# Optimization experiments

Measured on AMD Instinct MI355X. Metric: run time of the kernel, lower is better.

Reference implementation:

```python
import jax, jax.numpy as jnp
import numpy as np

NUM_EXPERTS = 8
GROUP_SIZE = 2
NUM_GROUPS = NUM_EXPERTS // GROUP_SIZE
NUM_SLOTS = 128
HIDDEN = 2048
D_FF = int(HIDDEN * 4 * (2.0 / 3.0))  # 5461
BATCH = 4
SEQ = 2048
BS = BATCH * SEQ


def setup_inputs() -> dict:
    key = jax.random.key(0)
    k0, k1, k2, k3 = jax.random.split(key, 4)
    x = jax.random.normal(k0, (BS, HIDDEN), dtype=jnp.float32)
    router_weights = jax.random.normal(k1, (BS, NUM_EXPERTS), dtype=jnp.float32)
    up_w = jax.random.normal(k2, (NUM_GROUPS, HIDDEN, D_FF), dtype=jnp.float32) * np.float32(1.0 / np.sqrt(HIDDEN))
    up_b = jnp.zeros((NUM_GROUPS, D_FF), dtype=jnp.float32)
    down_w = jax.random.normal(k3, (NUM_EXPERTS, D_FF, HIDDEN), dtype=jnp.float32) * np.float32(1.0 / np.sqrt(D_FF))
    down_b = jnp.zeros((NUM_EXPERTS, HIDDEN), dtype=jnp.float32)
    return {
        "x": x,
        "router_weights": router_weights,
        "up_w": up_w,
        "up_b": up_b,
        "down_w": down_w,
        "down_b": down_b,
        "batch_size": BATCH,
        "seq_len": SEQ,
    }


def reference(x, router_weights, up_w, up_b, down_w, down_b, batch_size, seq_len):
    # --- soft routing matrices (Soft-MoE; source raises NotImplementedError) ---
    h = router_weights                                   # (bs, E) routing logits
    dispatch = jax.nn.softmax(h, axis=0)                 # normalize over tokens per expert
    P = jnp.broadcast_to(dispatch[:, None, :], (h.shape[0], NUM_SLOTS, NUM_EXPERTS))  # (bs, k, E)
    G = jnp.full((NUM_SLOTS, NUM_EXPERTS), 1.0 / NUM_SLOTS, dtype=x.dtype)            # expert-choice combine (k, E)

    # --- dispatch: expert slot inputs ---
    tokens_for_expert = jnp.einsum('bke,bh->ekh', P, x)  # (E, k, hidden)

    # --- per-expert FFN (grouped up proj shared within each expert group) ---
    group_idx = np.arange(NUM_EXPERTS) // GROUP_SIZE     # static gather of shared up weights
    up_w_e = up_w[group_idx]                             # (E, hidden, d_ff)
    up_b_e = up_b[group_idx]                             # (E, d_ff)
    mid = jax.nn.silu(jnp.einsum('ekh,ehf->ekf', tokens_for_expert, up_w_e) + up_b_e[:, None, :])
    E_out = jnp.einsum('ekf,efh->ekh', mid, down_w) + down_b[:, None, :]  # (E, k, hidden)

    # --- combine (expert-choice branch): 'bs k e, k e, e k h -> bs h' ---
    y = jnp.einsum('bke,ke,ekh->bh', P, G, E_out)
    return y.reshape(batch_size, seq_len, HIDDEN)
```

## Files before the change

kernel.cpp:

```cpp
#include <hip/hip_runtime.h>

typedef float f4 __attribute__((ext_vector_type(4)));

#define HID 2048
#define DFF 5461
#define NE  8

#define WS_STATS 0
#define WS_T     64
#define WS_EO    16448

#define SC_TP 0
#define SC_MP 4194304
#define SC_EP 5592320

__device__ __forceinline__ void merge_ms(float& m, float& s, float mo, float so) {
  float mn = fmaxf(m, mo);
  s = s * __expf(m - mn) + so * __expf(mo - mn);
  m = mn;
}

__global__ __launch_bounds__(256) void k_stats(const float* __restrict__ rw,
                                               float* __restrict__ ws) {
  int e = blockIdx.x, tid = threadIdx.x;
  float m = -3.0e38f, s = 0.f;
#pragma unroll 4
  for (int r = 0; r < 32; r++) {
    float v = rw[(size_t)(r * 256 + tid) * NE + e];
    float mn = fmaxf(m, v);
    s = s * __expf(m - mn) + __expf(v - mn);
    m = mn;
  }
#pragma unroll
  for (int off = 32; off >= 1; off >>= 1) {
    float mo = __shfl_xor(m, off, 64);
    float so = __shfl_xor(s, off, 64);
    merge_ms(m, s, mo, so);
  }
  __shared__ float ml[4], sl[4];
  if ((tid & 63) == 0) { ml[tid >> 6] = m; sl[tid >> 6] = s; }
  __syncthreads();
  if (tid == 0) {
#pragma unroll
    for (int w = 1; w < 4; w++) merge_ms(m, s, ml[w], sl[w]);
    ws[WS_STATS + e] = m;
    ws[WS_STATS + 8 + e] = 1.f / s;
  }
}

__global__ __launch_bounds__(256) void k_tpart(const float* __restrict__ x,
                                               const float* __restrict__ rw,
                                               const float* __restrict__ ws,
                                               float* __restrict__ sc) {
  __shared__ f4 dv4[32][2];
  __shared__ f4 red[NE][128];
  int tid = threadIdx.x;
  int rc = blockIdx.y, b0 = rc * 32;
  if (tid < 64) {
    int row = tid >> 1, half = tid & 1;
    const float* rp = rw + (size_t)(b0 + row) * NE + half * 4;
    int e0 = half * 4;
    f4 d;
    d.x = __expf(rp[0] - ws[WS_STATS + e0 + 0]) * ws[WS_STATS + 8 + e0 + 0];
    d.y = __expf(rp[1] - ws[WS_STATS + e0 + 1]) * ws[WS_STATS + 8 + e0 + 1];
    d.z = __expf(rp[2] - ws[WS_STATS + e0 + 2]) * ws[WS_STATS + 8 + e0 + 2];
    d.w = __expf(rp[3] - ws[WS_STATS + e0 + 3]) * ws[WS_STATS + 8 + e0 + 3];
    dv4[row][half] = d;
  }
  __syncthreads();
  int col = tid & 127, rg = tid >> 7;
  int c4 = blockIdx.x * 128 + col;
  f4 acc[NE];
#pragma unroll
  for (int e = 0; e < NE; e++) acc[e] = (f4){0.f, 0.f, 0.f, 0.f};
  const f4* x4 = (const f4*)x;
#pragma unroll 4
  for (int r = 0; r < 16; r++) {
    int row = rg * 16 + r;
    f4 xv = __builtin_nontemporal_load(&x4[(size_t)(b0 + row) * 512 + c4]);
    f4 dlo = dv4[row][0], dhi = dv4[row][1];
    acc[0] += dlo.x * xv;
    acc[1] += dlo.y * xv;
    acc[2] += dlo.z * xv;
    acc[3] += dlo.w * xv;
    acc[4] += dhi.x * xv;
    acc[5] += dhi.y * xv;
    acc[6] += dhi.z * xv;
    acc[7] += dhi.w * xv;
  }
  if (rg) {
#pragma unroll
    for (int e = 0; e < NE; e++) red[e][col] = acc[e];
  }
  __syncthreads();
  if (!rg) {
    f4* o4 = (f4*)(sc + SC_TP);
#pragma unroll
    for (int e = 0; e < NE; e++)
      o4[(size_t)(rc * NE + e) * 512 + c4] = acc[e] + red[e][col];
  }
}

__global__ __launch_bounds__(256) void k_tred(const float* __restrict__ sc,
                                              float* __restrict__ ws) {
  __shared__ float red[8][32];
  int tid = threadIdx.x;
  int o = tid & 31, grp = tid >> 5;
  int i = blockIdx.x * 32 + o;
  float a = 0.f;
#pragma unroll 8
  for (int k = 0; k < 32; k++)
    a += sc[SC_TP + (size_t)(grp * 32 + k) * (NE * HID) + i];
  red[grp][o] = a;
  __syncthreads();
  if (tid < 32) {
    float s = 0.f;
#pragma unroll
    for (int g = 0; g < 8; g++) s += red[g][tid];
    ws[WS_T + blockIdx.x * 32 + tid] = s;
  }
}

__global__ __launch_bounds__(256) void k_midpart(const float* __restrict__ up_w,
                                                 const float* __restrict__ ws,
                                                 float* __restrict__ sc) {
  int fb = blockIdx.x, hc = blockIdx.y, g = blockIdx.z;
  int tid = threadIdx.x;
  __shared__ float t0[64], t1[64];
  int h0 = hc * 64;
  if (tid < 64) t0[tid] = ws[WS_T + (2 * g) * HID + h0 + tid];
  else if (tid < 128) t1[tid - 64] = ws[WS_T + (2 * g + 1) * HID + h0 + tid - 64];
  __syncthreads();
  int fA = fb * 512 + tid;
  int fB = fA + 256;
  bool hasB = fB < DFF;
  const float* wp = up_w + ((size_t)g * HID + h0) * DFF;
  float a0 = 0.f, a1 = 0.f, bb0 = 0.f, bb1 = 0.f;
#pragma unroll 8
  for (int h = 0; h < 64; h++) {
    float wA = __builtin_nontemporal_load(wp + (size_t)h * DFF + fA);
    float wB = hasB ? __builtin_nontemporal_load(wp + (size_t)h * DFF + fB) : 0.f;
    a0 += t0[h] * wA;
    a1 += t1[h] * wA;
    bb0 += t0[h] * wB;
    bb1 += t1[h] * wB;
  }
  float* mp = sc + SC_MP + (size_t)hc * NE * DFF;
  mp[(size_t)(2 * g) * DFF + fA] = a0;
  mp[(size_t)(2 * g + 1) * DFF + fA] = a1;
  if (hasB) {
    mp[(size_t)(2 * g) * DFF + fB] = bb0;
    mp[(size_t)(2 * g + 1) * DFF + fB] = bb1;
  }
}

__global__ __launch_bounds__(256) void k_eopart(const float* __restrict__ down_w,
                                                const float* __restrict__ up_b,
                                                const float* __restrict__ sc_mp,
                                                float* __restrict__ sc) {
  int hb = blockIdx.x, fc = blockIdx.y, e = blockIdx.z;
  int tid = threadIdx.x;
  int f0 = fc * 43;
  const f4* base4 = (const f4*)down_w + ((size_t)e * DFF + f0) * 512 + hb * 256 + tid;
  f4 w[8];
#pragma unroll
  for (int j = 0; j < 8; j++)
    w[j] = __builtin_nontemporal_load(&base4[(size_t)j * 512]);
  __shared__ float ml[4][43];
  int lane = tid & 63, wv = tid >> 6;
  if (lane < 43) {
    float a = up_b[(size_t)(e >> 1) * DFF + f0 + lane];
#pragma unroll 8
    for (int k = 0; k < 32; k++)
      a += sc_mp[SC_MP + (size_t)(k * NE + e) * DFF + f0 + lane];
    ml[wv][lane] = a / (1.f + __expf(-a));
  }
  f4 acc = (f4){0.f, 0.f, 0.f, 0.f};
  for (int blk = 0; blk < 5; blk++) {
#pragma unroll
    for (int j = 0; j < 8; j++) {
      int cur = blk * 8 + j;
      f4 c = w[j];
      int nxt = cur + 8;
      if (nxt < 43) w[j] = __builtin_nontemporal_load(&base4[(size_t)nxt * 512]);
      acc += ml[wv][cur] * c;
    }
  }
#pragma unroll
  for (int j = 0; j < 3; j++) acc += ml[wv][40 + j] * w[j];
  ((f4*)(sc + SC_EP))[(size_t)(fc * NE + e) * 512 + hb * 256 + tid] = acc;
}

__global__ __launch_bounds__(256) void k_eored(const float* __restrict__ sc,
                                               const float* __restrict__ down_b,
                                               float* __restrict__ ws) {
  __shared__ float red[8][32];
  int tid = threadIdx.x;
  int o = tid & 31, grp = tid >> 5;
  int i = blockIdx.x * 32 + o;
  float a = 0.f;
  for (int fc = grp; fc < 127; fc += 8)
    a += sc[SC_EP + (size_t)fc * (NE * HID) + i];
  red[grp][o] = a;
  __syncthreads();
  if (tid < 32) {
    int ii = blockIdx.x * 32 + tid;
    float s = down_b[ii];
#pragma unroll
    for (int g = 0; g < 8; g++) s += red[g][tid];
    ws[WS_EO + ii] = s;
  }
}

__global__ __launch_bounds__(256) void k_comb(const float* __restrict__ rw,
                                              const float* __restrict__ ws,
                                              float* __restrict__ y) {
  int tid = threadIdx.x;
  int b0 = blockIdx.x * 16;
  __shared__ float dvl[16][NE];
  if (tid < 128) {
    int tok = tid >> 3, e = tid & 7;
    dvl[tok][e] = __expf(rw[(size_t)(b0 + tok) * NE + e] - ws[WS_STATS + e]) *
                  ws[WS_STATS + 8 + e];
  }
  __syncthreads();
  const f4* eo4 = (const f4*)(ws + WS_EO);
  f4 ea[NE], eb[NE];
#pragma unroll
  for (int e = 0; e < NE; e++) {
    ea[e] = eo4[e * 512 + tid];
    eb[e] = eo4[e * 512 + 256 + tid];
  }
  f4* y4 = (f4*)y;
#pragma unroll 4
  for (int t = 0; t < 16; t++) {
    f4 o0 = (f4){0.f, 0.f, 0.f, 0.f};
    f4 o1 = (f4){0.f, 0.f, 0.f, 0.f};
#pragma unroll
    for (int e = 0; e < NE; e++) {
      float d = dvl[t][e];
      o0 += d * ea[e];
      o1 += d * eb[e];
    }
    __builtin_nontemporal_store(o0, &y4[(size_t)(b0 + t) * 512 + tid]);
    __builtin_nontemporal_store(o1, &y4[(size_t)(b0 + t) * 512 + 256 + tid]);
  }
}

extern "C" void kernel_launch(void* const* d_in, const int* in_sizes, int n_in,
                              void* d_out, int out_size, void* d_ws, size_t ws_size,
                              hipStream_t stream) {
  const float* x      = (const float*)d_in[0];
  const float* rw     = (const float*)d_in[1];
  const float* up_w   = (const float*)d_in[2];
  const float* up_b   = (const float*)d_in[3];
  const float* down_w = (const float*)d_in[4];
  const float* down_b = (const float*)d_in[5];
  float* y  = (float*)d_out;
  float* ws = (float*)d_ws;
  float* sc = y;

  hipLaunchKernelGGL(k_stats, dim3(8), dim3(256), 0, stream, rw, ws);
  hipLaunchKernelGGL(k_tpart, dim3(4, 256), dim3(256), 0, stream, x, rw, ws, sc);
  hipLaunchKernelGGL(k_tred, dim3(512), dim3(256), 0, stream, sc, ws);
  hipLaunchKernelGGL(k_midpart, dim3(11, 32, 4), dim3(256), 0, stream, up_w, ws, sc);
  hipLaunchKernelGGL(k_eopart, dim3(2, 127, 8), dim3(256), 0, stream, down_w, up_b, sc, sc);
  hipLaunchKernelGGL(k_eored, dim3(512), dim3(256), 0, stream, sc, down_b, ws);
  hipLaunchKernelGGL(k_comb, dim3(512), dim3(256), 0, stream, rw, ws, y);
}
```

Baseline: 143.3 us.

## Halve split-K partial counts and accumulate cross-partial reductions in double

k_tpart now gives each block 64 token rows split across four row groups instead of 32 rows across two, which halves the number of token partials written to scratch. k_midpart now covers 128 hidden rows per block instead of 64, which halves the up-projection partials. The reduction kernels read correspondingly fewer partials and the scratch offsets are compacted. Reductions in k_tred, k_eopart and k_eored now accumulate in double, which costs extra FP64 arithmetic in exchange for better accuracy.

```diff
diff --git a/kernel.cpp b/kernel.cpp
--- a/kernel.cpp
+++ b/kernel.cpp
@@ -6,13 +6,14 @@
 #define DFF 5461
 #define NE  8
 
-#define WS_STATS 0
-#define WS_T     64
-#define WS_EO    16448
+#define WS_M  0
+#define WS_IS 8
+#define WS_T  64
+#define WS_EO 16448
 
 #define SC_TP 0
-#define SC_MP 4194304
-#define SC_EP 5592320
+#define SC_MP 2097152
+#define SC_EP 2796288
 
 __device__ __forceinline__ void merge_ms(float& m, float& s, float mo, float so) {
   float mn = fmaxf(m, mo);
@@ -43,8 +44,8 @@
   if (tid == 0) {
 #pragma unroll
     for (int w = 1; w < 4; w++) merge_ms(m, s, ml[w], sl[w]);
-    ws[WS_STATS + e] = m;
-    ws[WS_STATS + 8 + e] = 1.f / s;
+    ws[WS_M + e] = m;
+    ws[WS_IS + e] = 1.f / s;
   }
 }
 
@@ -52,24 +53,24 @@
                                                const float* __restrict__ rw,
                                                const float* __restrict__ ws,
                                                float* __restrict__ sc) {
-  __shared__ f4 dv4[32][2];
-  __shared__ f4 red[NE][128];
-  int tid = threadIdx.x;
-  int rc = blockIdx.y, b0 = rc * 32;
-  if (tid < 64) {
+  __shared__ f4 dv4[64][2];
+  __shared__ f4 red[3][NE][64];
+  int tid = threadIdx.x;
+  int rc = blockIdx.y, b0 = rc * 64;
+  if (tid < 128) {
     int row = tid >> 1, half = tid & 1;
     const float* rp = rw + (size_t)(b0 + row) * NE + half * 4;
     int e0 = half * 4;
     f4 d;
-    d.x = __expf(rp[0] - ws[WS_STATS + e0 + 0]) * ws[WS_STATS + 8 + e0 + 0];
-    d.y = __expf(rp[1] - ws[WS_STATS + e0 + 1]) * ws[WS_STATS + 8 + e0 + 1];
-    d.z = __expf(rp[2] - ws[WS_STATS + e0 + 2]) * ws[WS_STATS + 8 + e0 + 2];
-    d.w = __expf(rp[3] - ws[WS_STATS + e0 + 3]) * ws[WS_STATS + 8 + e0 + 3];
+    d.x = __expf(rp[0] - ws[WS_M + e0 + 0]) * ws[WS_IS + e0 + 0];
+    d.y = __expf(rp[1] - ws[WS_M + e0 + 1]) * ws[WS_IS + e0 + 1];
+    d.z = __expf(rp[2] - ws[WS_M + e0 + 2]) * ws[WS_IS + e0 + 2];
+    d.w = __expf(rp[3] - ws[WS_M + e0 + 3]) * ws[WS_IS + e0 + 3];
     dv4[row][half] = d;
   }
   __syncthreads();
-  int col = tid & 127, rg = tid >> 7;
-  int c4 = blockIdx.x * 128 + col;
+  int col = tid & 63, rg = tid >> 6;
+  int c4 = blockIdx.x * 64 + col;
   f4 acc[NE];
 #pragma unroll
   for (int e = 0; e < NE; e++) acc[e] = (f4){0.f, 0.f, 0.f, 0.f};
@@ -90,14 +91,16 @@
   }
   if (rg) {
 #pragma unroll
-    for (int e = 0; e < NE; e++) red[e][col] = acc[e];
+    for (int e = 0; e < NE; e++) red[rg - 1][e][col] = acc[e];
   }
   __syncthreads();
   if (!rg) {
     f4* o4 = (f4*)(sc + SC_TP);
 #pragma unroll
-    for (int e = 0; e < NE; e++)
-      o4[(size_t)(rc * NE + e) * 512 + c4] = acc[e] + red[e][col];
+    for (int e = 0; e < NE; e++) {
+      f4 a = acc[e] + red[0][e][col] + red[1][e][col] + red[2][e][col];
+      o4[(size_t)(rc * NE + e) * 512 + c4] = a;
+    }
   }
 }
 
@@ -107,17 +110,18 @@
   int tid = threadIdx.x;
   int o = tid & 31, grp = tid >> 5;
   int i = blockIdx.x * 32 + o;
-  float a = 0.f;
-#pragma unroll 8
-  for (int k = 0; k < 32; k++)
-    a += sc[SC_TP + (size_t)(grp * 32 + k) * (NE * HID) + i];
-  red[grp][o] = a;
+  double a = 0.0;
+#pragma unroll 4
+  for (int k = 0; k < 16; k++)
+    a += (double)sc[SC_TP + (size_t)(grp * 16 + k) * (NE * HID) + i];
+  red[grp][o] = (float)a;
   __syncthreads();
   if (tid < 32) {
+    int ii = blockIdx.x * 32 + tid;
     float s = 0.f;
 #pragma unroll
     for (int g = 0; g < 8; g++) s += red[g][tid];
-    ws[WS_T + blockIdx.x * 32 + tid] = s;
+    ws[WS_T + ii] = s;
   }
 }
 
@@ -126,10 +130,10 @@
                                                  float* __restrict__ sc) {
   int fb = blockIdx.x, hc = blockIdx.y, g = blockIdx.z;
   int tid = threadIdx.x;
-  __shared__ float t0[64], t1[64];
-  int h0 = hc * 64;
-  if (tid < 64) t0[tid] = ws[WS_T + (2 * g) * HID + h0 + tid];
-  else if (tid < 128) t1[tid - 64] = ws[WS_T + (2 * g + 1) * HID + h0 + tid - 64];
+  __shared__ float t0[128], t1[128];
+  int h0 = hc * 128;
+  if (tid < 128) t0[tid] = ws[WS_T + (2 * g) * HID + h0 + tid];
+  else t1[tid - 128] = ws[WS_T + (2 * g + 1) * HID + h0 + tid - 128];
   __syncthreads();
   int fA = fb * 512 + tid;
   int fB = fA + 256;
@@ -137,7 +141,7 @@
   const float* wp = up_w + ((size_t)g * HID + h0) * DFF;
   float a0 = 0.f, a1 = 0.f, bb0 = 0.f, bb1 = 0.f;
 #pragma unroll 8
-  for (int h = 0; h < 64; h++) {
+  for (int h = 0; h < 128; h++) {
     float wA = __builtin_nontemporal_load(wp + (size_t)h * DFF + fA);
     float wB = hasB ? __builtin_nontemporal_load(wp + (size_t)h * DFF + fB) : 0.f;
     a0 += t0[h] * wA;
@@ -169,11 +173,12 @@
   __shared__ float ml[4][43];
   int lane = tid & 63, wv = tid >> 6;
   if (lane < 43) {
-    float a = up_b[(size_t)(e >> 1) * DFF + f0 + lane];
-#pragma unroll 8
-    for (int k = 0; k < 32; k++)
-      a += sc_mp[SC_MP + (size_t)(k * NE + e) * DFF + f0 + lane];
-    ml[wv][lane] = a / (1.f + __expf(-a));
+    double a = (double)up_b[(size_t)(e >> 1) * DFF + f0 + lane];
+#pragma unroll 4
+    for (int k = 0; k < 16; k++)
+      a += (double)sc_mp[SC_MP + (size_t)(k * NE + e) * DFF + f0 + lane];
+    float af = (float)a;
+    ml[wv][lane] = af / (1.f + __expf(-af));
   }
   f4 acc = (f4){0.f, 0.f, 0.f, 0.f};
   for (int blk = 0; blk < 5; blk++) {
@@ -198,10 +203,10 @@
   int tid = threadIdx.x;
   int o = tid & 31, grp = tid >> 5;
   int i = blockIdx.x * 32 + o;
-  float a = 0.f;
+  double a = 0.0;
   for (int fc = grp; fc < 127; fc += 8)
-    a += sc[SC_EP + (size_t)fc * (NE * HID) + i];
-  red[grp][o] = a;
+    a += (double)sc[SC_EP + (size_t)fc * (NE * HID) + i];
+  red[grp][o] = (float)a;
   __syncthreads();
   if (tid < 32) {
     int ii = blockIdx.x * 32 + tid;
@@ -220,8 +225,8 @@
   __shared__ float dvl[16][NE];
   if (tid < 128) {
     int tok = tid >> 3, e = tid & 7;
-    dvl[tok][e] = __expf(rw[(size_t)(b0 + tok) * NE + e] - ws[WS_STATS + e]) *
-                  ws[WS_STATS + 8 + e];
+    dvl[tok][e] = __expf(rw[(size_t)(b0 + tok) * NE + e] - ws[WS_M + e]) *
+                  ws[WS_IS + e];
   }
   __syncthreads();
   const f4* eo4 = (const f4*)(ws + WS_EO);
@@ -261,9 +266,9 @@
   float* sc = y;
 
   hipLaunchKernelGGL(k_stats, dim3(8), dim3(256), 0, stream, rw, ws);
-  hipLaunchKernelGGL(k_tpart, dim3(4, 256), dim3(256), 0, stream, x, rw, ws, sc);
+  hipLaunchKernelGGL(k_tpart, dim3(8, 128), dim3(256), 0, stream, x, rw, ws, sc);
   hipLaunchKernelGGL(k_tred, dim3(512), dim3(256), 0, stream, sc, ws);
-  hipLaunchKernelGGL(k_midpart, dim3(11, 32, 4), dim3(256), 0, stream, up_w, ws, sc);
+  hipLaunchKernelGGL(k_midpart, dim3(11, 16, 4), dim3(256), 0, stream, up_w, ws, sc);
   hipLaunchKernelGGL(k_eopart, dim3(2, 127, 8), dim3(256), 0, stream, down_w, up_b, sc, sc);
   hipLaunchKernelGGL(k_eored, dim3(512), dim3(256), 0, stream, sc, down_b, ws);
   hipLaunchKernelGGL(k_comb, dim3(512), dim3(256), 0, stream, rw, ws, y);
```

Measured after the change: 137.9 us. -3.8%, faster.
